# Optimization experiments

Measured on AMD Instinct MI355X. Metric: run time of the kernel, lower is better.

Reference implementation:

```python
import jax, jax.numpy as jnp
import numpy as np

B, S, D, H = 8, 1024, 768, 12
HEAD_DIM = D // H  # 64
# NOTE: original code divides scores by scaling=(head_dim)**-0.5, i.e. MULTIPLIES by sqrt(head_dim)
SCORE_SCALE = float(HEAD_DIM) ** 0.5


def setup_inputs() -> dict:
    key = jax.random.key(0)
    ks = jax.random.split(key, 9)
    std = 1.0 / np.sqrt(D)
    return {
        "x":  jax.random.normal(ks[0], (B, S, D), jnp.float32),
        "Wq": jax.random.normal(ks[1], (H, D, D), jnp.float32) * std,
        "bq": jax.random.normal(ks[2], (H, D), jnp.float32) * std,
        "Wk": jax.random.normal(ks[3], (H, D, D), jnp.float32) * std,
        "bk": jax.random.normal(ks[4], (H, D), jnp.float32) * std,
        "Wv": jax.random.normal(ks[5], (H, D, D), jnp.float32) * std,
        "bv": jax.random.normal(ks[6], (H, D), jnp.float32) * std,
        "Wp": jax.random.normal(ks[7], (H * D, D), jnp.float32) * (1.0 / np.sqrt(H * D)),
        "bp": jax.random.normal(ks[8], (D,), jnp.float32) * std,
    }


def reference(x, Wq, bq, Wk, bk, Wv, bv, Wp, bp):
    # Per-head full-width projections, batched over the head axis h.
    q = jnp.einsum('bsd,hde->bhse', x, Wq) + bq[None, :, None, :]  # [B,H,S,D]
    k = jnp.einsum('bsd,hde->bhse', x, Wk) + bk[None, :, None, :]
    v = jnp.einsum('bsd,hde->bhse', x, Wv) + bv[None, :, None, :]
    scores = jnp.einsum('bhse,bhte->bhst', q, k) * SCORE_SCALE    # [B,H,S,S]
    attn = jax.nn.softmax(scores, axis=-1)
    o = jnp.einsum('bhst,bhte->bhse', attn, v)                     # [B,H,S,D]
    # concat heads along last dim (head-major order matches torch.cat)
    o = jnp.transpose(o, (0, 2, 1, 3)).reshape(B, S, H * D)        # [B,S,H*D]
    return o @ Wp + bp                                             # [B,S,D]
```

## Files before the change

### kernel.cpp

```cpp
#include <hip/hip_runtime.h>


typedef __attribute__((ext_vector_type(8))) short bf16x8;
typedef __attribute__((ext_vector_type(4))) float fx4;

#define NB 8
#define NS 1024
#define ND 768
#define NH 12

__device__ __forceinline__ unsigned short f2bf(float x) {
    unsigned int u = __float_as_uint(x);
    u += 0x7fffu + ((u >> 16) & 1u);
    return (unsigned short)(u >> 16);
}
__device__ __forceinline__ float bf2f(unsigned short h) {
    return __uint_as_float(((unsigned int)h) << 16);
}

__device__ __forceinline__ void gll16(const void* g, void* l) {
    __builtin_amdgcn_global_load_lds(
        (const __attribute__((address_space(1))) void*)g,
        (__attribute__((address_space(3))) void*)l, 16, 0, 0);
}

__device__ __forceinline__ void split_body(const float* __restrict__ in,
                                           unsigned short* __restrict__ hi,
                                           unsigned short* __restrict__ lo, int i) {
    float4 v = ((const float4*)in)[i];
    ushort4 h, l;
    h.x = f2bf(v.x); l.x = f2bf(v.x - bf2f(h.x));
    h.y = f2bf(v.y); l.y = f2bf(v.y - bf2f(h.y));
    h.z = f2bf(v.z); l.z = f2bf(v.z - bf2f(h.z));
    h.w = f2bf(v.w); l.w = f2bf(v.w - bf2f(h.w));
    ((ushort4*)hi)[i] = h;
    ((ushort4*)lo)[i] = l;
}

template<int NTERMS, class Epi>
__device__ __forceinline__ void gemm_core64(
    char* __restrict__ smem,
    const unsigned short* __restrict__ Ah, const unsigned short* __restrict__ Al, int lda,
    const unsigned short* __restrict__ Bh, const unsigned short* __restrict__ Bl, int ldb,
    int K, Epi epi)
{
    constexpr int TILE = 16384;

    const int t = threadIdx.x;
    const int lane = t & 63;
    const int w = t >> 6;
    const int wm = (w >> 1) << 6;
    const int wn = (w & 1) << 6;
    const int lr = lane & 15;
    const int lg = lane >> 4;

    const int l3 = lane >> 3;
    const int cs = (lane & 7) ^ l3;
    const int ldsw = w << 12;

    const long gsA = (long)(w * 32 + l3) * lda * 2 + cs * 16;
    const long gsB = (long)(w * 32 + l3) * ldb * 2 + cs * 16;
    const long giA = (long)lda * 16;
    const long giB = (long)ldb * 16;

    const char* pAh = (const char*)Ah;
    const char* pBh = (const char*)Bh;
    const char* pAl = (const char*)Al;
    const char* pBl = (const char*)Bl;
    char* smA  = smem;
    char* smB  = smem + TILE;
    char* smA2 = smem + ((NTERMS == 3) ? 2 * TILE : 0);
    char* smB2 = smem + ((NTERMS == 3) ? 3 * TILE : TILE);

    int rowA[4], rowB[4];
    #pragma unroll
    for (int i = 0; i < 4; i++) {
        rowA[i] = (wm + (i << 4) + lr) << 6;
        rowB[i] = (wn + (i << 4) + lr) << 6;
    }
    const int lr7 = lr & 7;

    fx4 acc[4][4] = {};

    for (int k0 = 0; k0 < K; k0 += 64) {
        const long kb2 = (long)k0 * 2;
        __syncthreads();
        #pragma unroll
        for (int ii = 0; ii < 4; ii++) {
            const int lo = ldsw + (ii << 10);
            gll16(pAh + gsA + ii * giA + kb2, smA + lo);
            gll16(pBh + gsB + ii * giB + kb2, smB + lo);
            if constexpr (NTERMS == 3) {
                gll16(pAl + gsA + ii * giA + kb2, smA2 + lo);
                gll16(pBl + gsB + ii * giB + kb2, smB2 + lo);
            }
        }
        __syncthreads();

        #pragma unroll
        for (int kk = 0; kk < 2; kk++) {
            const int pc = (((kk << 2) + lg) ^ lr7) << 3;
            bf16x8 fa[4], fb[4], fa2[4], fb2[4];
            #pragma unroll
            for (int i = 0; i < 4; i++) {
                fa[i] = *(const bf16x8*)((const unsigned short*)smA + rowA[i] + pc);
                fb[i] = *(const bf16x8*)((const unsigned short*)smB + rowB[i] + pc);
            }
            if constexpr (NTERMS == 3) {
                #pragma unroll
                for (int i = 0; i < 4; i++) {
                    fa2[i] = *(const bf16x8*)((const unsigned short*)smA2 + rowA[i] + pc);
                    fb2[i] = *(const bf16x8*)((const unsigned short*)smB2 + rowB[i] + pc);
                }
            }
            #pragma unroll
            for (int i = 0; i < 4; i++)
                #pragma unroll
                for (int j = 0; j < 4; j++) {
                    acc[i][j] = __builtin_amdgcn_mfma_f32_16x16x32_bf16(fa[i], fb[j], acc[i][j], 0, 0, 0);
                    if constexpr (NTERMS == 3) {
                        acc[i][j] = __builtin_amdgcn_mfma_f32_16x16x32_bf16(fa[i], fb2[j], acc[i][j], 0, 0, 0);
                        acc[i][j] = __builtin_amdgcn_mfma_f32_16x16x32_bf16(fa2[i], fb[j], acc[i][j], 0, 0, 0);
                    }
                }
        }
    }

    #pragma unroll
    for (int i = 0; i < 4; i++)
        #pragma unroll
        for (int j = 0; j < 4; j++)
            #pragma unroll
            for (int r = 0; r < 4; r++)
                epi(wm + (i << 4) + (lg << 2) + r, wn + (j << 4) + lr, acc[i][j][r]);
}

__device__ __forceinline__ void softmax_row_core(const float* __restrict__ rp,
                                                 unsigned short* __restrict__ drow,
                                                 int lane) {
    const float4* src = (const float4*)rp + (lane << 2);
    float v[16];
    #pragma unroll
    for (int i = 0; i < 4; i++) {
        float4 a = src[i];
        v[i * 4 + 0] = a.x; v[i * 4 + 1] = a.y; v[i * 4 + 2] = a.z; v[i * 4 + 3] = a.w;
    }
    float m = v[0];
    #pragma unroll
    for (int i = 1; i < 16; i++) m = fmaxf(m, v[i]);
    #pragma unroll
    for (int o = 32; o > 0; o >>= 1) m = fmaxf(m, __shfl_xor(m, o));
    float s = 0.f, p[16];
    #pragma unroll
    for (int i = 0; i < 16; i++) { p[i] = __expf((v[i] - m) * 8.0f); s += p[i]; }
    #pragma unroll
    for (int o = 32; o > 0; o >>= 1) s += __shfl_xor(s, o);
    float inv = 1.0f / s;
    unsigned int wrd[8];
    #pragma unroll
    for (int i = 0; i < 8; i++) {
        unsigned int u0 = f2bf(p[2 * i] * inv);
        unsigned int u1 = f2bf(p[2 * i + 1] * inv);
        wrd[i] = u0 | (u1 << 16);
    }
    uint4* dst = (uint4*)(drow + (lane << 4));
    dst[0] = make_uint4(wrd[0], wrd[1], wrd[2], wrd[3]);
    dst[1] = make_uint4(wrd[4], wrd[5], wrd[6], wrd[7]);
}

__global__ void k_su_a(
    const float* __restrict__ x, unsigned short* __restrict__ xh, unsigned short* __restrict__ xl,
    const float* __restrict__ Wq, unsigned short* __restrict__ Wqh, unsigned short* __restrict__ Wql,
    const float* __restrict__ Wk, unsigned short* __restrict__ Wkh, unsigned short* __restrict__ Wkl,
    const float* __restrict__ bq, float* __restrict__ rk,
    const float* __restrict__ Wv, unsigned short* __restrict__ Wvb,
    const float* __restrict__ Wp, unsigned short* __restrict__ WpT)
{
    __shared__ float tile[64][65];
    const int bx = blockIdx.x;
    if (bx < 6144) {
        split_body(x, xh, xl, bx * 256 + threadIdx.x);
    } else if (bx < 13056) {
        split_body(Wq, Wqh, Wql, (bx - 6144) * 256 + threadIdx.x);
    } else if (bx < 19968) {
        split_body(Wk, Wkh, Wkl, (bx - 13056) * 256 + threadIdx.x);
    } else if (bx < 22272) {
        const int idx = bx - 19968;
        const int h = idx / 192;
        const int d = (idx % 192) * 4 + ((int)threadIdx.x >> 6);
        const int lane = threadIdx.x & 63;
        const float4* row = (const float4*)(Wk + ((long)h * ND + d) * ND);
        const float4* bv4 = (const float4*)(bq + h * ND);
        float acc = 0.f;
        #pragma unroll
        for (int i = 0; i < 3; i++) {
            float4 a = row[lane + (i << 6)];
            float4 b = bv4[lane + (i << 6)];
            acc += a.x * b.x + a.y * b.y + a.z * b.z + a.w * b.w;
        }
        #pragma unroll
        for (int o = 32; o > 0; o >>= 1) acc += __shfl_xor(acc, o);
        if (lane == 0) rk[h * ND + d] = acc;
    } else if (bx < 29184) {
        int i = (bx - 22272) * 256 + threadIdx.x;
        float4 v = ((const float4*)Wv)[i];
        ushort4 h;
        h.x = f2bf(v.x); h.y = f2bf(v.y); h.z = f2bf(v.z); h.w = f2bf(v.w);
        ((ushort4*)Wvb)[i] = h;
    } else {
        const int idx = bx - 29184;
        const int c0 = (idx % 12) * 64;
        const int r0 = ((idx / 12) % 12) * 64;
        const long zo = (long)(idx / 144) * (ND * ND);
        const float* in = Wp + zo;
        unsigned short* oh = WpT + zo;
        const int tc = threadIdx.x & 63, t4 = threadIdx.x >> 6;
        #pragma unroll
        for (int i = 0; i < 16; i++) {
            int r = (i << 2) + t4;
            tile[r][tc] = in[(long)(r0 + r) * ND + c0 + tc];
        }
        __syncthreads();
        #pragma unroll
        for (int i = 0; i < 16; i++) {
            int c = (i << 2) + t4;
            oh[(long)(c0 + c) * ND + r0 + tc] = f2bf(tile[tc][c]);
        }
    }
}

__global__ __launch_bounds__(256, 2) void k_su_b(
    const unsigned short* __restrict__ Wkh, const unsigned short* __restrict__ Wkl,
    const unsigned short* __restrict__ Wqh, const unsigned short* __restrict__ Wql,
    unsigned short* __restrict__ MTh, unsigned short* __restrict__ MTl,
    const float* __restrict__ x, const float* __restrict__ rk, float* __restrict__ w_all,
    const unsigned short* __restrict__ WpT, const unsigned short* __restrict__ Wvb,
    unsigned short* __restrict__ NTo, const float* __restrict__ bv,
    float* __restrict__ s_all)
{
    __shared__ __align__(16) char smem[65536];
    const int bx = blockIdx.x;
    if (bx < 432) {
        const int tid = (bx & 7) * 54 + (bx >> 3);
        const int n0 = (tid % 6) << 7;
        const int m0 = ((tid / 6) % 6) << 7;
        const long hw = (long)(tid / 36) * (ND * ND);
        unsigned short* oh = MTh + hw + (long)m0 * ND + n0;
        unsigned short* ol = MTl + hw + (long)m0 * ND + n0;
        gemm_core64<3>(smem, Wkh + hw + (long)m0 * ND, Wkl + hw + (long)m0 * ND, ND,
                       Wqh + hw + (long)n0 * ND, Wql + hw + (long)n0 * ND, ND, ND,
                       [=](int r, int c, float v) {
                           unsigned short hh = f2bf(v);
                           oh[r * ND + c] = hh;
                           ol[r * ND + c] = f2bf(v - bf2f(hh));
                       });
    } else if (bx < 2480) {
        float* srk = (float*)smem;
        for (int i = threadIdx.x; i < NH * ND; i += 256) srk[i] = rk[i];
        __syncthreads();
        const int row = (bx - 432) * 4 + ((int)threadIdx.x >> 6);
        const int lane = threadIdx.x & 63;
        const float4* xr = (const float4*)(x + (long)row * ND);
        float4 xa[3];
        #pragma unroll
        for (int i = 0; i < 3; i++) xa[i] = xr[lane + (i << 6)];
        for (int h = 0; h < NH; h++) {
            const float* r = srk + h * ND;
            float acc = 0.f;
            #pragma unroll
            for (int i = 0; i < 3; i++) {
                int e = (lane + (i << 6)) << 2;
                acc += xa[i].x * r[e] + xa[i].y * r[e + 1]
                     + xa[i].z * r[e + 2] + xa[i].w * r[e + 3];
            }
            #pragma unroll
            for (int o = 32; o > 0; o >>= 1) acc += __shfl_xor(acc, o);
            if (lane == 0) w_all[h * (NB * NS) + row] = acc;
        }
    } else if (bx < 2912) {
        const int b2 = bx - 2480;
        const int tid = (b2 & 7) * 54 + (b2 >> 3);
        const int n0 = (tid % 6) << 7;
        const int m0 = ((tid / 6) % 6) << 7;
        const long hw = (long)(tid / 36) * (ND * ND);
        unsigned short* o = NTo + hw + (long)m0 * ND + n0;
        gemm_core64<1>(smem, WpT + hw + (long)m0 * ND, nullptr, ND,
                       Wvb + hw + (long)n0 * ND, nullptr, ND, ND,
                       [=](int r, int c, float v) { o[r * ND + c] = f2bf(v); });
    } else {
        const int idx = bx - 2912;
        const int h = idx / 192;
        const int j = (idx % 192) * 4 + ((int)threadIdx.x >> 6);
        const int lane = threadIdx.x & 63;
        const ushort4* row = (const ushort4*)(WpT + ((long)h * ND + j) * ND);
        const float* bvh = bv + h * ND;
        float acc = 0.f;
        #pragma unroll
        for (int i = 0; i < 3; i++) {
            int c = lane + (i << 6);
            ushort4 u = row[c];
            int e = c << 2;
            acc += bf2f(u.x) * bvh[e] + bf2f(u.y) * bvh[e + 1]
                 + bf2f(u.z) * bvh[e + 2] + bf2f(u.w) * bvh[e + 3];
        }
        #pragma unroll
        for (int o = 32; o > 0; o >>= 1) acc += __shfl_xor(acc, o);
        if (lane == 0) s_all[h * ND + j] = acc;
    }
}


__global__ __launch_bounds__(256, 2) void k_G0(
    const unsigned short* __restrict__ xh, const unsigned short* __restrict__ xl,
    const unsigned short* __restrict__ MTh, const unsigned short* __restrict__ MTl,
    unsigned short* __restrict__ Gh, unsigned short* __restrict__ Gl)
{
    __shared__ __align__(16) char smem[65536];
    const int bx = blockIdx.x;
    const int xcd = bx & 7, idx = bx >> 3;
    const int m0 = (xcd * 8 + idx / 6) << 7;
    const int n0 = (idx % 6) << 7;
    unsigned short* oh = Gh + (long)m0 * ND + n0;
    unsigned short* ol = Gl + (long)m0 * ND + n0;
    gemm_core64<3>(smem, xh + (long)m0 * ND, xl + (long)m0 * ND, ND,
                   MTh + (long)n0 * ND, MTl + (long)n0 * ND, ND, ND,
                   [=](int r, int c, float v) {
                       unsigned short hh = f2bf(v);
                       oh[(long)r * ND + c] = hh;
                       ol[(long)r * ND + c] = f2bf(v - bf2f(hh));
                   });
}

__global__ __launch_bounds__(256, 2) void k_SZ(
    const unsigned short* __restrict__ Gh, const unsigned short* __restrict__ Gl,
    const unsigned short* __restrict__ xh, const unsigned short* __restrict__ xl,
    const float* __restrict__ wv, float* __restrict__ Sc,
    const unsigned short* __restrict__ NTh, const float* __restrict__ sh,
    unsigned short* __restrict__ ZT)
{
    __shared__ __align__(16) char smem[65536];
    const int bx = blockIdx.x;
    if (bx < 512) {
        const int bl = bx & 7, idx = bx >> 3;
        const int m0 = (idx >> 3) << 7;
        const int n0 = (idx & 7) << 7;
        const long ao = ((long)bl * NS + m0) * ND;
        const long bo = ((long)bl * NS + n0) * ND;
        const float* ww = wv + bl * NS + n0;
        float* out = Sc + ((long)bl * NS + m0) * NS + n0;
        gemm_core64<3>(smem, Gh + ao, Gl + ao, ND, xh + bo, xl + bo, ND, ND,
                       [=](int r, int c, float v) { out[(long)r * NS + c] = v + ww[c]; });
    } else {
        const int g = bx - 512;
        const int xcd = g & 7, idx = g >> 3;
        const int m0 = (xcd * 8 + idx / 6) << 7;
        const int n0 = (idx % 6) << 7;
        const int bl = m0 >> 10;
        const int s0 = m0 & (NS - 1);
        unsigned short* zt = ZT + (long)bl * (ND * NS);
        gemm_core64<1>(smem, xh + (long)m0 * ND, nullptr, ND,
                       NTh + (long)n0 * ND, nullptr, ND, ND,
                       [=](int r, int c, float v) {
                           zt[(long)(n0 + c) * NS + s0 + r] = f2bf(v + sh[n0 + c]);
                       });
    }
}

__global__ __launch_bounds__(256, 2) void k_SMG1(
    const float* __restrict__ Sc, unsigned short* __restrict__ Pp,
    const unsigned short* __restrict__ xh, const unsigned short* __restrict__ xl,
    const unsigned short* __restrict__ MTh, const unsigned short* __restrict__ MTl,
    unsigned short* __restrict__ Gh, unsigned short* __restrict__ Gl)
{
    __shared__ __align__(16) char smem[65536];
    const int bx = blockIdx.x;
    if (bx < 2048) {
        int row = bx * 4 + ((int)threadIdx.x >> 6);
        int lane = threadIdx.x & 63;
        softmax_row_core(Sc + (long)row * NS, Pp + (long)row * NS, lane);
    } else {
        const int g = bx - 2048;
        const int xcd = g & 7, idx = g >> 3;
        const int m0 = (xcd * 8 + idx / 6) << 7;
        const int n0 = (idx % 6) << 7;
        unsigned short* oh = Gh + (long)m0 * ND + n0;
        unsigned short* ol = Gl + (long)m0 * ND + n0;
        gemm_core64<3>(smem, xh + (long)m0 * ND, xl + (long)m0 * ND, ND,
                       MTh + (long)n0 * ND, MTl + (long)n0 * ND, ND, ND,
                       [=](int r, int c, float v) {
                           unsigned short hh = f2bf(v);
                           oh[(long)r * ND + c] = hh;
                           ol[(long)r * ND + c] = f2bf(v - bf2f(hh));
                       });
    }
}

template<int MODE>
__global__ __launch_bounds__(256, 2) void k_PVSZ1(
    const unsigned short* __restrict__ Pp, const unsigned short* __restrict__ ZTr,
    const float* __restrict__ bp, float* __restrict__ outp,
    const unsigned short* __restrict__ Gh, const unsigned short* __restrict__ Gl,
    const unsigned short* __restrict__ xh, const unsigned short* __restrict__ xl,
    const float* __restrict__ wv, float* __restrict__ Sc,
    const unsigned short* __restrict__ NTh, const float* __restrict__ sh,
    unsigned short* __restrict__ ZTw)
{
    __shared__ __align__(16) char smem[65536];
    const int bx = blockIdx.x;
    if (bx < 384) {
        const int bl = bx & 7, idx = bx >> 3;
        const int m0 = (idx / 6) << 7;
        const int n0 = (idx % 6) << 7;
        const unsigned short* A = Pp + ((long)bl * NS + m0) * NS;
        const unsigned short* B = ZTr + (long)bl * (ND * NS) + (long)n0 * NS;
        float* o = outp + ((long)bl * NS + m0) * ND + n0;
        const float* bi = bp + n0;
        gemm_core64<1>(smem, A, nullptr, NS, B, nullptr, NS, NS,
                       [=](int r, int c, float v) {
                           float* d = o + (long)r * ND + c;
                           if constexpr (MODE == 0) *d = v + bi[c];
                           else *d += v;
                       });
    } else if (bx < 896) {
        const int b2 = bx - 384;
        const int bl = b2 & 7, idx = b2 >> 3;
        const int m0 = (idx >> 3) << 7;
        const int n0 = (idx & 7) << 7;
        const long ao = ((long)bl * NS + m0) * ND;
        const long bo = ((long)bl * NS + n0) * ND;
        const float* ww = wv + bl * NS + n0;
        float* out = Sc + ((long)bl * NS + m0) * NS + n0;
        gemm_core64<3>(smem, Gh + ao, Gl + ao, ND, xh + bo, xl + bo, ND, ND,
                       [=](int r, int c, float v) { out[(long)r * NS + c] = v + ww[c]; });
    } else {
        const int g = bx - 896;
        const int xcd = g & 7, idx = g >> 3;
        const int m0 = (xcd * 8 + idx / 6) << 7;
        const int n0 = (idx % 6) << 7;
        const int bl = m0 >> 10;
        const int s0 = m0 & (NS - 1);
        unsigned short* zt = ZTw + (long)bl * (ND * NS);
        gemm_core64<1>(smem, xh + (long)m0 * ND, nullptr, ND,
                       NTh + (long)n0 * ND, nullptr, ND, ND,
                       [=](int r, int c, float v) {
                           zt[(long)(n0 + c) * NS + s0 + r] = f2bf(v + sh[n0 + c]);
                       });
    }
}


extern "C" void kernel_launch(void* const* d_in, const int* in_sizes, int n_in,
                              void* d_out, int out_size, void* d_ws, size_t ws_size,
                              hipStream_t stream) {
    (void)in_sizes; (void)n_in; (void)out_size; (void)ws_size;
    const float* x  = (const float*)d_in[0];
    const float* Wq = (const float*)d_in[1];
    const float* bq = (const float*)d_in[2];
    const float* Wk = (const float*)d_in[3];
    const float* bk = (const float*)d_in[4];  (void)bk;
    const float* Wv = (const float*)d_in[5];
    const float* bv = (const float*)d_in[6];
    const float* Wp = (const float*)d_in[7];
    const float* bp = (const float*)d_in[8];

    const size_t nx  = (size_t)NB * NS * ND;
    const size_t nw  = (size_t)NH * ND * ND;
    const size_t nwh = (size_t)ND * ND;
    const size_t PPE = (size_t)NB * NS * NS;
    const size_t ZTE = (size_t)NB * NS * ND;

    char* p = (char*)d_ws;
    auto alloc = [&](size_t bytes) -> void* {
        void* r = (void*)p;
        p += (bytes + 255) & ~(size_t)255;
        return r;
    };
    unsigned short* xh   = (unsigned short*)alloc(nx * 2);
    unsigned short* xl   = (unsigned short*)alloc(nx * 2);
    unsigned short* MTh  = (unsigned short*)alloc(nw * 2);
    unsigned short* MTl  = (unsigned short*)alloc(nw * 2);
    unsigned short* NTb  = (unsigned short*)alloc(nw * 2);
    float*          rk   = (float*)alloc((size_t)NH * ND * 4);
    float*          s_all= (float*)alloc((size_t)NH * ND * 4);
    float*          w_all= (float*)alloc((size_t)NH * NB * NS * 4);
    float*          Sc = (float*)alloc(PPE * 4);
    unsigned short* Gh = (unsigned short*)alloc(nx * 2);
    unsigned short* Gl = (unsigned short*)alloc(nx * 2);
    unsigned short* Pp = (unsigned short*)alloc(PPE * 2);
    unsigned short* ZT = (unsigned short*)alloc(2 * ZTE * 2);
    unsigned short* Wqh = (unsigned short*)Sc;
    unsigned short* Wql = Wqh + nw;
    unsigned short* Wkh = Wql + nw;
    unsigned short* Wkl = Wkh + nw;
    unsigned short* Wvb = Wkl + nw;
    unsigned short* WpT = Wvb + nw;

    k_su_a<<<30912, 256, 0, stream>>>(x, xh, xl, Wq, Wqh, Wql, Wk, Wkh, Wkl,
                                      bq, rk, Wv, Wvb, Wp, WpT);
    k_su_b<<<5216, 256, 0, stream>>>(Wkh, Wkl, Wqh, Wql, MTh, MTl, x, rk, w_all,
                                     WpT, Wvb, NTb, bv, s_all);

    k_G0<<<384, 256, 0, stream>>>(xh, xl, MTh, MTl, Gh, Gl);
    k_SZ<<<896, 256, 0, stream>>>(Gh, Gl, xh, xl, w_all, Sc, NTb, s_all, ZT);
    for (int h = 0; h < NH; h++) {
        const int hn = h + 1;
        const bool hasG = hn < NH;
        const int hs = hasG ? hn : 0;
        k_SMG1<<<hasG ? 2432 : 2048, 256, 0, stream>>>(
            Sc, Pp, xh, xl, MTh + (long)hs * nwh, MTl + (long)hs * nwh, Gh, Gl);
        unsigned short* ZTr = ZT + (size_t)(h & 1) * ZTE;
        unsigned short* ZTw = ZT + (size_t)(hn & 1) * ZTE;
        const int grid = hasG ? 1280 : 384;
        if (h == 0)
            k_PVSZ1<0><<<grid, 256, 0, stream>>>(
                Pp, ZTr, bp, (float*)d_out, Gh, Gl, xh, xl,
                w_all + (long)hs * NB * NS, Sc, NTb + (long)hs * nwh,
                s_all + hs * ND, ZTw);
        else
            k_PVSZ1<1><<<grid, 256, 0, stream>>>(
                Pp, ZTr, bp, (float*)d_out, Gh, Gl, xh, xl,
                w_all + (long)hs * NB * NS, Sc, NTb + (long)hs * nwh,
                s_all + hs * ND, ZTw);
    }
}
```

Measured before the change: 1.363 ms.

## Defer per-head weight-product GEMMs into the per-head softmax kernels

The setup kernel used to compute the weight-product matrices (Wk·Wq and WpT·Wv) for all 12 heads up front. Now only heads 0 and 1 are computed during setup. The product for head h+2 is computed by extra blocks appended to the softmax/G kernel of head h, so this work overlaps with the per-head pipeline instead of sitting in a serial setup phase. This requires moving the bf16 weight copies out of the Sc alias into dedicated workspace buffers, which adds memory footprint and launches more blocks per iteration.

```diff
diff --git a/kernel.cpp b/kernel.cpp
--- a/kernel.cpp
+++ b/kernel.cpp
@@ -229,36 +229,17 @@
     }
 }
 
-__global__ __launch_bounds__(256, 2) void k_su_b(
-    const unsigned short* __restrict__ Wkh, const unsigned short* __restrict__ Wkl,
-    const unsigned short* __restrict__ Wqh, const unsigned short* __restrict__ Wql,
-    unsigned short* __restrict__ MTh, unsigned short* __restrict__ MTl,
+__global__ __launch_bounds__(256) void k_su_y(
     const float* __restrict__ x, const float* __restrict__ rk, float* __restrict__ w_all,
-    const unsigned short* __restrict__ WpT, const unsigned short* __restrict__ Wvb,
-    unsigned short* __restrict__ NTo, const float* __restrict__ bv,
+    const unsigned short* __restrict__ WpT, const float* __restrict__ bv,
     float* __restrict__ s_all)
 {
-    __shared__ __align__(16) char smem[65536];
-    const int bx = blockIdx.x;
-    if (bx < 432) {
-        const int tid = (bx & 7) * 54 + (bx >> 3);
-        const int n0 = (tid % 6) << 7;
-        const int m0 = ((tid / 6) % 6) << 7;
-        const long hw = (long)(tid / 36) * (ND * ND);
-        unsigned short* oh = MTh + hw + (long)m0 * ND + n0;
-        unsigned short* ol = MTl + hw + (long)m0 * ND + n0;
-        gemm_core64<3>(smem, Wkh + hw + (long)m0 * ND, Wkl + hw + (long)m0 * ND, ND,
-                       Wqh + hw + (long)n0 * ND, Wql + hw + (long)n0 * ND, ND, ND,
-                       [=](int r, int c, float v) {
-                           unsigned short hh = f2bf(v);
-                           oh[r * ND + c] = hh;
-                           ol[r * ND + c] = f2bf(v - bf2f(hh));
-                       });
-    } else if (bx < 2480) {
-        float* srk = (float*)smem;
+    __shared__ float srk[NH * ND];
+    const int bx = blockIdx.x;
+    if (bx < 2048) {
         for (int i = threadIdx.x; i < NH * ND; i += 256) srk[i] = rk[i];
         __syncthreads();
-        const int row = (bx - 432) * 4 + ((int)threadIdx.x >> 6);
+        const int row = bx * 4 + ((int)threadIdx.x >> 6);
         const int lane = threadIdx.x & 63;
         const float4* xr = (const float4*)(x + (long)row * ND);
         float4 xa[3];
@@ -277,18 +258,8 @@
             for (int o = 32; o > 0; o >>= 1) acc += __shfl_xor(acc, o);
             if (lane == 0) w_all[h * (NB * NS) + row] = acc;
         }
-    } else if (bx < 2912) {
-        const int b2 = bx - 2480;
-        const int tid = (b2 & 7) * 54 + (b2 >> 3);
-        const int n0 = (tid % 6) << 7;
-        const int m0 = ((tid / 6) % 6) << 7;
-        const long hw = (long)(tid / 36) * (ND * ND);
-        unsigned short* o = NTo + hw + (long)m0 * ND + n0;
-        gemm_core64<1>(smem, WpT + hw + (long)m0 * ND, nullptr, ND,
-                       Wvb + hw + (long)n0 * ND, nullptr, ND, ND,
-                       [=](int r, int c, float v) { o[r * ND + c] = f2bf(v); });
     } else {
-        const int idx = bx - 2912;
+        const int idx = bx - 2048;
         const int h = idx / 192;
         const int j = (idx % 192) * 4 + ((int)threadIdx.x >> 6);
         const int lane = threadIdx.x & 63;
@@ -306,6 +277,38 @@
         #pragma unroll
         for (int o = 32; o > 0; o >>= 1) acc += __shfl_xor(acc, o);
         if (lane == 0) s_all[h * ND + j] = acc;
+    }
+}
+
+__global__ __launch_bounds__(256, 2) void k_su_x(
+    const unsigned short* __restrict__ Wkh, const unsigned short* __restrict__ Wkl,
+    const unsigned short* __restrict__ Wqh, const unsigned short* __restrict__ Wql,
+    unsigned short* __restrict__ MTh, unsigned short* __restrict__ MTl,
+    const unsigned short* __restrict__ WpT, const unsigned short* __restrict__ Wvb,
+    unsigned short* __restrict__ NTo)
+{
+    __shared__ __align__(16) char smem[65536];
+    const int bx = blockIdx.x;
+    const int part = bx / 36, t = bx % 36;
+    const int n0 = (t % 6) << 7;
+    const int m0 = (t / 6) << 7;
+    if (part < 2) {
+        const long hw = (long)part * (ND * ND);
+        unsigned short* oh = MTh + hw + (long)m0 * ND + n0;
+        unsigned short* ol = MTl + hw + (long)m0 * ND + n0;
+        gemm_core64<3>(smem, Wkh + hw + (long)m0 * ND, Wkl + hw + (long)m0 * ND, ND,
+                       Wqh + hw + (long)n0 * ND, Wql + hw + (long)n0 * ND, ND, ND,
+                       [=](int r, int c, float v) {
+                           unsigned short hh = f2bf(v);
+                           oh[r * ND + c] = hh;
+                           ol[r * ND + c] = f2bf(v - bf2f(hh));
+                       });
+    } else {
+        const long hw = (long)(part - 2) * (ND * ND);
+        unsigned short* o = NTo + hw + (long)m0 * ND + n0;
+        gemm_core64<1>(smem, WpT + hw + (long)m0 * ND, nullptr, ND,
+                       Wvb + hw + (long)n0 * ND, nullptr, ND, ND,
+                       [=](int r, int c, float v) { o[r * ND + c] = f2bf(v); });
     }
 }
 
@@ -369,8 +372,13 @@
 __global__ __launch_bounds__(256, 2) void k_SMG1(
     const float* __restrict__ Sc, unsigned short* __restrict__ Pp,
     const unsigned short* __restrict__ xh, const unsigned short* __restrict__ xl,
-    const unsigned short* __restrict__ MTh, const unsigned short* __restrict__ MTl,
-    unsigned short* __restrict__ Gh, unsigned short* __restrict__ Gl)
+    const unsigned short* __restrict__ MTgh, const unsigned short* __restrict__ MTgl,
+    unsigned short* __restrict__ Gh, unsigned short* __restrict__ Gl,
+    const unsigned short* __restrict__ Wkh_p, const unsigned short* __restrict__ Wkl_p,
+    const unsigned short* __restrict__ Wqh_p, const unsigned short* __restrict__ Wql_p,
+    unsigned short* __restrict__ MTph, unsigned short* __restrict__ MTpl,
+    const unsigned short* __restrict__ WpT_p, const unsigned short* __restrict__ Wvb_p,
+    unsigned short* __restrict__ NTp)
 {
     __shared__ __align__(16) char smem[65536];
     const int bx = blockIdx.x;
@@ -378,7 +386,7 @@
         int row = bx * 4 + ((int)threadIdx.x >> 6);
         int lane = threadIdx.x & 63;
         softmax_row_core(Sc + (long)row * NS, Pp + (long)row * NS, lane);
-    } else {
+    } else if (bx < 2432) {
         const int g = bx - 2048;
         const int xcd = g & 7, idx = g >> 3;
         const int m0 = (xcd * 8 + idx / 6) << 7;
@@ -386,12 +394,33 @@
         unsigned short* oh = Gh + (long)m0 * ND + n0;
         unsigned short* ol = Gl + (long)m0 * ND + n0;
         gemm_core64<3>(smem, xh + (long)m0 * ND, xl + (long)m0 * ND, ND,
-                       MTh + (long)n0 * ND, MTl + (long)n0 * ND, ND, ND,
+                       MTgh + (long)n0 * ND, MTgl + (long)n0 * ND, ND, ND,
                        [=](int r, int c, float v) {
                            unsigned short hh = f2bf(v);
                            oh[(long)r * ND + c] = hh;
                            ol[(long)r * ND + c] = f2bf(v - bf2f(hh));
                        });
+    } else if (bx < 2468) {
+        const int t = bx - 2432;
+        const int n0 = (t % 6) << 7;
+        const int m0 = (t / 6) << 7;
+        unsigned short* oh = MTph + (long)m0 * ND + n0;
+        unsigned short* ol = MTpl + (long)m0 * ND + n0;
+        gemm_core64<3>(smem, Wkh_p + (long)m0 * ND, Wkl_p + (long)m0 * ND, ND,
+                       Wqh_p + (long)n0 * ND, Wql_p + (long)n0 * ND, ND, ND,
+                       [=](int r, int c, float v) {
+                           unsigned short hh = f2bf(v);
+                           oh[r * ND + c] = hh;
+                           ol[r * ND + c] = f2bf(v - bf2f(hh));
+                       });
+    } else {
+        const int t = bx - 2468;
+        const int n0 = (t % 6) << 7;
+        const int m0 = (t / 6) << 7;
+        unsigned short* o = NTp + (long)m0 * ND + n0;
+        gemm_core64<1>(smem, WpT_p + (long)m0 * ND, nullptr, ND,
+                       Wvb_p + (long)n0 * ND, nullptr, ND, ND,
+                       [=](int r, int c, float v) { o[r * ND + c] = f2bf(v); });
     }
 }
 
@@ -483,22 +512,22 @@
     float*          rk   = (float*)alloc((size_t)NH * ND * 4);
     float*          s_all= (float*)alloc((size_t)NH * ND * 4);
     float*          w_all= (float*)alloc((size_t)NH * NB * NS * 4);
-    float*          Sc = (float*)alloc(PPE * 4);
-    unsigned short* Gh = (unsigned short*)alloc(nx * 2);
-    unsigned short* Gl = (unsigned short*)alloc(nx * 2);
-    unsigned short* Pp = (unsigned short*)alloc(PPE * 2);
-    unsigned short* ZT = (unsigned short*)alloc(2 * ZTE * 2);
-    unsigned short* Wqh = (unsigned short*)Sc;
-    unsigned short* Wql = Wqh + nw;
-    unsigned short* Wkh = Wql + nw;
-    unsigned short* Wkl = Wkh + nw;
-    unsigned short* Wvb = Wkl + nw;
-    unsigned short* WpT = Wvb + nw;
+    unsigned short* Wqh  = (unsigned short*)alloc(nw * 2);
+    unsigned short* Wql  = (unsigned short*)alloc(nw * 2);
+    unsigned short* Wkh  = (unsigned short*)alloc(nw * 2);
+    unsigned short* Wkl  = (unsigned short*)alloc(nw * 2);
+    unsigned short* Wvb  = (unsigned short*)alloc(nw * 2);
+    unsigned short* WpT  = (unsigned short*)alloc(nw * 2);
+    float*          Sc   = (float*)alloc(PPE * 4);
+    unsigned short* Gh   = (unsigned short*)alloc(nx * 2);
+    unsigned short* Gl   = (unsigned short*)alloc(nx * 2);
+    unsigned short* Pp   = (unsigned short*)alloc(PPE * 2);
+    unsigned short* ZT   = (unsigned short*)alloc(2 * ZTE * 2);
 
     k_su_a<<<30912, 256, 0, stream>>>(x, xh, xl, Wq, Wqh, Wql, Wk, Wkh, Wkl,
                                       bq, rk, Wv, Wvb, Wp, WpT);
-    k_su_b<<<5216, 256, 0, stream>>>(Wkh, Wkl, Wqh, Wql, MTh, MTl, x, rk, w_all,
-                                     WpT, Wvb, NTb, bv, s_all);
+    k_su_y<<<4352, 256, 0, stream>>>(x, rk, w_all, WpT, bv, s_all);
+    k_su_x<<<144, 256, 0, stream>>>(Wkh, Wkl, Wqh, Wql, MTh, MTl, WpT, Wvb, NTb);
 
     k_G0<<<384, 256, 0, stream>>>(xh, xl, MTh, MTl, Gh, Gl);
     k_SZ<<<896, 256, 0, stream>>>(Gh, Gl, xh, xl, w_all, Sc, NTb, s_all, ZT);
@@ -506,8 +535,18 @@
         const int hn = h + 1;
         const bool hasG = hn < NH;
         const int hs = hasG ? hn : 0;
-        k_SMG1<<<hasG ? 2432 : 2048, 256, 0, stream>>>(
-            Sc, Pp, xh, xl, MTh + (long)hs * nwh, MTl + (long)hs * nwh, Gh, Gl);
+        const int hp = h + 2;
+        const bool hasP = hp < NH;
+        const int hpp = hasP ? hp : 0;
+        const int gridS = hasP ? 2504 : (hasG ? 2432 : 2048);
+        k_SMG1<<<gridS, 256, 0, stream>>>(
+            Sc, Pp, xh, xl,
+            MTh + (long)hs * nwh, MTl + (long)hs * nwh, Gh, Gl,
+            Wkh + (long)hpp * nwh, Wkl + (long)hpp * nwh,
+            Wqh + (long)hpp * nwh, Wql + (long)hpp * nwh,
+            MTh + (long)hpp * nwh, MTl + (long)hpp * nwh,
+            WpT + (long)hpp * nwh, Wvb + (long)hpp * nwh,
+            NTb + (long)hpp * nwh);
         unsigned short* ZTr = ZT + (size_t)(h & 1) * ZTE;
         unsigned short* ZTw = ZT + (size_t)(hn & 1) * ZTE;
         const int grid = hasG ? 1280 : 384;
```

Result: slower. 1.492 ms (+9.4%).
